# Kernel optimization log

Measured on AMD Instinct MI355X. Metric: run time of the kernel, lower is better.

The kernel has to match this reference:

```python
import jax, jax.numpy as jnp
import numpy as np
import math

D_MODEL = 1024
NUM_HEADS = 16
HEAD_DIM = D_MODEL // NUM_HEADS


def _xavier(key, out_f, in_f):
    limit = math.sqrt(6.0 / (in_f + out_f))
    return jax.random.uniform(key, (out_f, in_f), jnp.float32, -limit, limit)


def ternarize(w):
    # abs-mean threshold -> {-1, 0, +1}
    abs_mean = jnp.mean(jnp.abs(w))
    return jnp.where(jnp.abs(w) > abs_mean, jnp.sign(w), jnp.zeros_like(w))


def setup_inputs() -> dict:
    key = jax.random.key(0)
    kq, kk, kv, kwq, kwk, kwv, kwo = jax.random.split(key, 7)
    B, S = 2, 2048
    return {
        "query": jax.random.normal(kq, (B, S, D_MODEL), jnp.float32),
        "key": jax.random.normal(kk, (B, S, D_MODEL), jnp.float32),
        "value": jax.random.normal(kv, (B, S, D_MODEL), jnp.float32),
        "w_q": _xavier(kwq, D_MODEL, D_MODEL),
        "w_k": _xavier(kwk, D_MODEL, D_MODEL),
        "w_v": _xavier(kwv, D_MODEL, D_MODEL),
        "w_o": _xavier(kwo, D_MODEL, D_MODEL),
    }


def reference(query, key, value, w_q, w_k, w_v, w_o):
    B, S, _ = query.shape
    # ternary projections (F.linear: x @ W.T)
    q = query @ ternarize(w_q).T
    k = key @ ternarize(w_k).T
    v = value @ ternarize(w_v).T
    # [B, H, S, Dh]
    q = q.reshape(B, S, NUM_HEADS, HEAD_DIM).transpose(0, 2, 1, 3)
    k = k.reshape(B, -1, NUM_HEADS, HEAD_DIM).transpose(0, 2, 1, 3)
    v = v.reshape(B, -1, NUM_HEADS, HEAD_DIM).transpose(0, 2, 1, 3)
    scores = jnp.einsum("bhqd,bhkd->bhqk", q, k) / math.sqrt(HEAD_DIM)
    probs = jax.nn.softmax(scores, axis=-1)
    out = jnp.einsum("bhqk,bhkd->bhqd", probs, v)
    out = out.transpose(0, 2, 1, 3).reshape(B, S, D_MODEL)
    return out @ ternarize(w_o).T
```

## Files before the change

### kernel.cpp

```cpp
#include <hip/hip_runtime.h>
#include <cstdint>
#include <cstddef>

typedef __bf16 bfloat;
typedef __bf16 bf16x8 __attribute__((ext_vector_type(8)));
typedef __bf16 bf16x4 __attribute__((ext_vector_type(4)));
typedef float  f32x4  __attribute__((ext_vector_type(4)));

static constexpr int D  = 1024;
static constexpr int S  = 2048;
static constexpr int B  = 2;
static constexpr int H  = 16;
static constexpr int DH = 64;
static constexpr int M  = B * S;
static constexpr int WMAT_N = 1024 * 1024;

#define MFMA_BF16(a, b, c) __builtin_amdgcn_mfma_f32_16x16x32_bf16((a), (b), (c), 0, 0, 0)

__device__ __forceinline__ void gl_lds16(const void* g, void* l) {
  __builtin_amdgcn_global_load_lds(
      (const __attribute__((address_space(1))) void*)g,
      (__attribute__((address_space(3))) void*)l, 16, 0, 0);
}

__global__ void prep_kernel(const float* __restrict__ w0, const float* __restrict__ w1,
                            const float* __restrict__ w2, const float* __restrict__ w3,
                            const float* __restrict__ qx, const float* __restrict__ kx,
                            const float* __restrict__ vx, bfloat* __restrict__ qhi,
                            bfloat* __restrict__ qlo, bfloat* __restrict__ khi,
                            bfloat* __restrict__ klo, bfloat* __restrict__ vhi,
                            double* __restrict__ sums) {
  const int y = blockIdx.y;
  if (y < 4) {
    const float* w = (y == 0) ? w0 : (y == 1) ? w1 : (y == 2) ? w2 : w3;
    const float4* w4 = (const float4*)w;
    double s = 0.0;
    for (int i = blockIdx.x * blockDim.x + threadIdx.x; i < (WMAT_N / 4);
         i += gridDim.x * blockDim.x) {
      float4 v = w4[i];
      s += (double)fabsf(v.x) + (double)fabsf(v.y) + (double)fabsf(v.z) + (double)fabsf(v.w);
    }
    for (int off = 1; off < 64; off <<= 1) s += __shfl_xor(s, off, 64);
    __shared__ double ps[4];
    if ((threadIdx.x & 63) == 0) ps[threadIdx.x >> 6] = s;
    __syncthreads();
    if (threadIdx.x == 0) atomicAdd(&sums[y], ps[0] + ps[1] + ps[2] + ps[3]);
  } else {
    const int z = y - 4;
    const float* x = (z == 0) ? qx : (z == 1) ? kx : vx;
    bfloat* hi = (z == 0) ? qhi : (z == 1) ? khi : vhi;
    bfloat* lo = (z == 0) ? qlo : (z == 1) ? klo : nullptr;
    const int n8 = M * D / 8;
    const float4* x4 = (const float4*)x;
    for (int i = blockIdx.x * blockDim.x + threadIdx.x; i < n8;
         i += gridDim.x * blockDim.x) {
      float4 a = x4[2 * i], b = x4[2 * i + 1];
      float f[8] = {a.x, a.y, a.z, a.w, b.x, b.y, b.z, b.w};
      bf16x8 h;
#pragma unroll
      for (int j = 0; j < 8; j++) h[j] = (bfloat)f[j];
      *(bf16x8*)&hi[(size_t)i * 8] = h;
      if (z < 2) {
        bf16x8 l;
#pragma unroll
        for (int j = 0; j < 8; j++) l[j] = (bfloat)(f[j] - (float)h[j]);
        *(bf16x8*)&lo[(size_t)i * 8] = l;
      }
    }
  }
}

__global__ void tern_kernel(const float* __restrict__ w0, const float* __restrict__ w1,
                            const float* __restrict__ w2, const float* __restrict__ w3,
                            bfloat* __restrict__ o0, bfloat* __restrict__ o1,
                            bfloat* __restrict__ o2, bfloat* __restrict__ o3,
                            const double* __restrict__ sums) {
  int z = blockIdx.y;
  const float* w = (z == 0) ? w0 : (z == 1) ? w1 : (z == 2) ? w2 : w3;
  bfloat* o = (z == 0) ? o0 : (z == 1) ? o1 : (z == 2) ? o2 : o3;
  double thr = sums[z] * (1.0 / (double)WMAT_N);
  const float4* w4 = (const float4*)w;
  for (int i = blockIdx.x * blockDim.x + threadIdx.x; i < (WMAT_N / 4);
       i += gridDim.x * blockDim.x) {
    float4 v = w4[i];
    bf16x4 r;
    r[0] = (bfloat)(((double)fabsf(v.x) > thr) ? (v.x > 0.f ? 1.f : -1.f) : 0.f);
    r[1] = (bfloat)(((double)fabsf(v.y) > thr) ? (v.y > 0.f ? 1.f : -1.f) : 0.f);
    r[2] = (bfloat)(((double)fabsf(v.z) > thr) ? (v.z > 0.f ? 1.f : -1.f) : 0.f);
    r[3] = (bfloat)(((double)fabsf(v.w) > thr) ? (v.w > 0.f ? 1.f : -1.f) : 0.f);
    *(bf16x4*)&o[(size_t)i * 4] = r;
  }
}

__global__ __launch_bounds__(256) void qkv_gemm(
    const bfloat* __restrict__ xqh, const bfloat* __restrict__ xql,
    const bfloat* __restrict__ xkh, const bfloat* __restrict__ xkl,
    const bfloat* __restrict__ xvh, const bfloat* __restrict__ wqt,
    const bfloat* __restrict__ wkt, const bfloat* __restrict__ wvt,
    bfloat* __restrict__ qmh, bfloat* __restrict__ qml,
    bfloat* __restrict__ kmh, bfloat* __restrict__ kml, bfloat* __restrict__ vtr) {
  constexpr int K = D;
  constexpr int N = D;
  __shared__ __align__(16) bfloat As0[128 * 64];
  __shared__ __align__(16) bfloat As1[128 * 64];
  __shared__ __align__(16) bfloat Ws[128 * 64];

  const int z = blockIdx.z;
  const bfloat *A0, *A1 = nullptr, *Wm;
  bfloat *Oh = nullptr, *Ol = nullptr;
  float scale = 1.f;
  bool split;
  if (z == 0) {
    A0 = xqh; A1 = xql; Wm = wqt; Oh = qmh; Ol = qml;
    scale = 0.18033688f;
    split = true;
  } else if (z == 1) {
    A0 = xkh; A1 = xkl; Wm = wkt; Oh = kmh; Ol = kml; split = true;
  } else {
    A0 = xvh; Wm = wvt; split = false;
  }

  const int t = threadIdx.x;
  const int w = t >> 6, lane = t & 63;
  const int quad = lane >> 4, l16 = lane & 15;
  const int wm = w >> 1, wn = w & 1;
  const int m0 = blockIdx.y * 128, n0 = blockIdx.x * 128;

  f32x4 acc[4][4] = {};

  const int srr = lane >> 3;
  const int spc = lane & 7;

  for (int kk = 0; kk < K; kk += 64) {
#pragma unroll
    for (int g = 0; g < 4; g++) {
      int row = w * 32 + g * 8 + srr;
      int cl = spc ^ (row & 7);
      int lo = (w * 32 + g * 8) * 64;
      gl_lds16(A0 + (size_t)(m0 + row) * K + kk + cl * 8, As0 + lo);
      if (split) gl_lds16(A1 + (size_t)(m0 + row) * K + kk + cl * 8, As1 + lo);
      gl_lds16(Wm + (size_t)(n0 + row) * K + kk + cl * 8, Ws + lo);
    }
    __syncthreads();

#pragma unroll
    for (int kidx = 0; kidx < 2; kidx++) {
      bf16x8 bfrag[4], afrag[4];
#pragma unroll
      for (int nt = 0; nt < 4; nt++) {
        int r = wn * 64 + nt * 16 + l16;
        bfrag[nt] = *(const bf16x8*)&Ws[r * 64 + (((kidx * 4 + quad) ^ (r & 7)) * 8)];
      }
#pragma unroll
      for (int mt = 0; mt < 4; mt++) {
        int r = wm * 64 + mt * 16 + l16;
        afrag[mt] = *(const bf16x8*)&As0[r * 64 + (((kidx * 4 + quad) ^ (r & 7)) * 8)];
      }
#pragma unroll
      for (int mt = 0; mt < 4; mt++)
#pragma unroll
        for (int nt = 0; nt < 4; nt++)
          acc[mt][nt] = MFMA_BF16(afrag[mt], bfrag[nt], acc[mt][nt]);
      if (split) {
#pragma unroll
        for (int mt = 0; mt < 4; mt++) {
          int r = wm * 64 + mt * 16 + l16;
          afrag[mt] = *(const bf16x8*)&As1[r * 64 + (((kidx * 4 + quad) ^ (r & 7)) * 8)];
        }
#pragma unroll
        for (int mt = 0; mt < 4; mt++)
#pragma unroll
          for (int nt = 0; nt < 4; nt++)
            acc[mt][nt] = MFMA_BF16(afrag[mt], bfrag[nt], acc[mt][nt]);
      }
    }
    __syncthreads();
  }

#pragma unroll
  for (int mt = 0; mt < 4; mt++) {
#pragma unroll
    for (int nt = 0; nt < 4; nt++) {
      const int row = m0 + wm * 64 + mt * 16 + quad * 4;
      const int col = n0 + wn * 64 + nt * 16 + l16;
      if (split) {
#pragma unroll
        for (int rg = 0; rg < 4; rg++) {
          float vv = acc[mt][nt][rg] * scale;
          size_t idx = (size_t)(row + rg) * N + col;
          bfloat hh = (bfloat)vv;
          Oh[idx] = hh;
          Ol[idx] = (bfloat)(vv - (float)hh);
        }
      } else {
        int bb = row >> 11, s = row & (S - 1);
        bf16x4 pk;
#pragma unroll
        for (int rg = 0; rg < 4; rg++) pk[rg] = (bfloat)acc[mt][nt][rg];
        *(bf16x4*)&vtr[(size_t)bb * D * S + (size_t)col * S + s] = pk;
      }
    }
  }
}

__global__ __launch_bounds__(256, 4) void gemm_wo(const bfloat* __restrict__ A,
                                                  const bfloat* __restrict__ Wm,
                                                  float* __restrict__ Cf) {
  constexpr int K = D;
  constexpr int N = D;
  __shared__ __align__(16) bfloat As[64 * 32];
  __shared__ __align__(16) bfloat Ws[64 * 32];

  const int t = threadIdx.x;
  const int w = t >> 6, lane = t & 63;
  const int quad = lane >> 4, l16 = lane & 15;
  const int wm = w >> 1, wn = w & 1;
  const int m0 = blockIdx.y * 64, n0 = blockIdx.x * 64;

  f32x4 acc[2][2] = {};

  const int sr = w * 16 + (lane >> 2);
  const int sc = (lane & 3) ^ ((sr >> 1) & 3);

  const bfloat* pA = A + (size_t)(m0 + sr) * K + sc * 8;
  const bfloat* pW = Wm + (size_t)(n0 + sr) * K + sc * 8;
  const int ldso = w * 16 * 32;

  for (int kk = 0; kk < K; kk += 32) {
    gl_lds16(pA + kk, As + ldso);
    gl_lds16(pW + kk, Ws + ldso);
    __syncthreads();

    bf16x8 af[2], bf[2];
#pragma unroll
    for (int i = 0; i < 2; i++) {
      int ar = wm * 32 + i * 16 + l16;
      af[i] = *(const bf16x8*)&As[ar * 32 + ((quad ^ ((ar >> 1) & 3)) * 8)];
      int br = wn * 32 + i * 16 + l16;
      bf[i] = *(const bf16x8*)&Ws[br * 32 + ((quad ^ ((br >> 1) & 3)) * 8)];
    }
#pragma unroll
    for (int mt = 0; mt < 2; mt++)
#pragma unroll
      for (int nt = 0; nt < 2; nt++)
        acc[mt][nt] = MFMA_BF16(af[mt], bf[nt], acc[mt][nt]);
    __syncthreads();
  }

#pragma unroll
  for (int mt = 0; mt < 2; mt++) {
#pragma unroll
    for (int nt = 0; nt < 2; nt++) {
      const int row = m0 + wm * 32 + mt * 16 + quad * 4;
      const int col = n0 + wn * 32 + nt * 16 + l16;
#pragma unroll
      for (int rg = 0; rg < 4; rg++) Cf[(size_t)(row + rg) * N + col] = acc[mt][nt][rg];
    }
  }
}

__global__ __launch_bounds__(256) void flash_kernel(
    const bfloat* __restrict__ qh, const bfloat* __restrict__ ql,
    const bfloat* __restrict__ kh, const bfloat* __restrict__ kl,
    const bfloat* __restrict__ vt, bfloat* __restrict__ outp) {
  __shared__ __align__(16) bfloat Kh[64 * 64];
  __shared__ __align__(16) bfloat Kl[64 * 64];
  __shared__ __align__(16) bfloat Vt[64 * 64];
  __shared__ __align__(16) bfloat Pm[64 * 64];

  const int t = threadIdx.x;
  const int w = t >> 6, lane = t & 63;
  const int quad = lane >> 4, l16 = lane & 15;
  const int b = blockIdx.z, h = blockIdx.y;
  const int q0 = blockIdx.x * 64;
  const size_t base = (size_t)b * S * D + (size_t)h * DH;
  const size_t vbase = (size_t)b * D * S + (size_t)h * DH * S;

  const int ssr = lane >> 3;
  const int spc = lane & 7;

  bf16x8 ones;
#pragma unroll
  for (int j = 0; j < 8; j++) ones[j] = (bfloat)1.f;

#pragma unroll
  for (int g = 0; g < 2; g++) {
    int r = w * 16 + g * 8 + ssr;
    int c = spc ^ (r & 7);
    int lo = (w * 16 + g * 8) * 64;
    gl_lds16(qh + base + (size_t)(q0 + r) * D + c * 8, Kh + lo);
    gl_lds16(ql + base + (size_t)(q0 + r) * D + c * 8, Kl + lo);
  }
  __syncthreads();
  bf16x8 qhf[2], qlf[2];
  {
    int row = w * 16 + l16;
#pragma unroll
    for (int s2 = 0; s2 < 2; s2++) {
      qhf[s2] = *(const bf16x8*)&Kh[row * 64 + (((s2 * 4 + quad) ^ (l16 & 7)) * 8)];
      qlf[s2] = *(const bf16x8*)&Kl[row * 64 + (((s2 * 4 + quad) ^ (l16 & 7)) * 8)];
    }
  }
  __syncthreads();

  f32x4 Oa[4] = {};
  f32x4 La = {};
  float m_i = -3.0e38f;

  for (int k0 = 0; k0 < S; k0 += 64) {
#pragma unroll
    for (int g = 0; g < 2; g++) {
      int r = w * 16 + g * 8 + ssr;
      int c = spc ^ (r & 7);
      int lo = (w * 16 + g * 8) * 64;
      gl_lds16(kh + base + (size_t)(k0 + r) * D + c * 8, Kh + lo);
      gl_lds16(kl + base + (size_t)(k0 + r) * D + c * 8, Kl + lo);
      gl_lds16(vt + vbase + (size_t)r * S + k0 + c * 8, Vt + lo);
    }
    __syncthreads();

    f32x4 sf[4];
#pragma unroll
    for (int mt = 0; mt < 4; mt++) {
      f32x4 a = {};
      int krow = mt * 16 + l16;
#pragma unroll
      for (int s2 = 0; s2 < 2; s2++) {
        bf16x8 bh = *(const bf16x8*)&Kh[krow * 64 + (((s2 * 4 + quad) ^ (l16 & 7)) * 8)];
        bf16x8 bl = *(const bf16x8*)&Kl[krow * 64 + (((s2 * 4 + quad) ^ (l16 & 7)) * 8)];
        a = MFMA_BF16(bh, qhf[s2], a);
        a = MFMA_BF16(bl, qhf[s2], a);
        a = MFMA_BF16(bh, qlf[s2], a);
      }
      sf[mt] = a;
    }

    float mm = sf[0][0];
#pragma unroll
    for (int mt = 0; mt < 4; mt++)
#pragma unroll
      for (int rg = 0; rg < 4; rg++) mm = fmaxf(mm, sf[mt][rg]);
    mm = fmaxf(mm, __shfl_xor(mm, 16, 64));
    mm = fmaxf(mm, __shfl_xor(mm, 32, 64));
    if (__ballot(mm > m_i)) {
      float mnew = fmaxf(m_i, mm);
      float alpha = exp2f(m_i - mnew);
      m_i = mnew;
#pragma unroll
      for (int mt = 0; mt < 4; mt++) Oa[mt] *= alpha;
      La *= alpha;
    }
#pragma unroll
    for (int mt = 0; mt < 4; mt++)
#pragma unroll
      for (int rg = 0; rg < 4; rg++) sf[mt][rg] = exp2f(sf[mt][rg] - m_i);

#pragma unroll
    for (int mt = 0; mt < 4; mt++) {
      bf16x4 pk;
#pragma unroll
      for (int rg = 0; rg < 4; rg++) pk[rg] = (bfloat)sf[mt][rg];
      int g16 = (mt * 2 + (quad >> 1)) ^ (l16 & 7);
      *(bf16x4*)&Pm[(w * 16 + l16) * 64 + g16 * 8 + (quad & 1) * 4] = pk;
    }

#pragma unroll
    for (int s2 = 0; s2 < 2; s2++) {
      bf16x8 pb = *(const bf16x8*)&Pm[(w * 16 + l16) * 64 +
                                      (((s2 * 4 + quad) ^ (l16 & 7)) * 8)];
#pragma unroll
      for (int mt = 0; mt < 4; mt++) {
        int vrow = mt * 16 + l16;
        bf16x8 va = *(const bf16x8*)&Vt[vrow * 64 + (((s2 * 4 + quad) ^ (l16 & 7)) * 8)];
        Oa[mt] = MFMA_BF16(va, pb, Oa[mt]);
      }
      La = MFMA_BF16(ones, pb, La);
    }
    __syncthreads();
  }

  float inv = 1.0f / La[0];
  const int qrow = q0 + w * 16 + l16;
#pragma unroll
  for (int mt = 0; mt < 4; mt++) {
    bf16x4 ov;
#pragma unroll
    for (int rg = 0; rg < 4; rg++) ov[rg] = (bfloat)(Oa[mt][rg] * inv);
    *(bf16x4*)&outp[base + (size_t)qrow * D + mt * 16 + quad * 4] = ov;
  }
}

extern "C" void kernel_launch(void* const* d_in, const int* in_sizes, int n_in,
                              void* d_out, int out_size, void* d_ws, size_t ws_size,
                              hipStream_t stream) {
  const float* q_in = (const float*)d_in[0];
  const float* k_in = (const float*)d_in[1];
  const float* v_in = (const float*)d_in[2];
  const float* wq = (const float*)d_in[3];
  const float* wk = (const float*)d_in[4];
  const float* wv = (const float*)d_in[5];
  const float* wo = (const float*)d_in[6];
  float* outp = (float*)d_out;
  char* ws = (char*)d_ws;

  constexpr size_t WBYTES = (size_t)WMAT_N * 2;
  constexpr size_t XBYTES = (size_t)M * D * 2;
  size_t off = 0;
  double* sums = (double*)(ws + off); off += 256;
  bfloat* wqt = (bfloat*)(ws + off); off += WBYTES;
  bfloat* wkt = (bfloat*)(ws + off); off += WBYTES;
  bfloat* wvt = (bfloat*)(ws + off); off += WBYTES;
  bfloat* wot = (bfloat*)(ws + off); off += WBYTES;
  bfloat* xqh = (bfloat*)(ws + off); off += XBYTES;
  bfloat* xql = (bfloat*)(ws + off); off += XBYTES;
  bfloat* xkh = (bfloat*)(ws + off); off += XBYTES;
  bfloat* xkl = (bfloat*)(ws + off); off += XBYTES;
  bfloat* xvh = (bfloat*)(ws + off); off += XBYTES;
  bfloat* qmh = (bfloat*)(ws + off); off += XBYTES;
  bfloat* qml = (bfloat*)(ws + off); off += XBYTES;
  bfloat* kmh = (bfloat*)(ws + off); off += XBYTES;
  bfloat* kml = (bfloat*)(ws + off); off += XBYTES;
  bfloat* vtr = (bfloat*)(ws + off); off += XBYTES;
  bfloat* attn = xqh;

  hipMemsetAsync(sums, 0, 4 * sizeof(double), stream);
  prep_kernel<<<dim3(256, 7), 256, 0, stream>>>(
      wq, wk, wv, wo, q_in, k_in, v_in, xqh, xql, xkh, xkl, xvh, sums);
  tern_kernel<<<dim3(128, 4), 256, 0, stream>>>(wq, wk, wv, wo, wqt, wkt, wvt, wot, sums);
  qkv_gemm<<<dim3(D / 128, M / 128, 3), 256, 0, stream>>>(
      xqh, xql, xkh, xkl, xvh, wqt, wkt, wvt, qmh, qml, kmh, kml, vtr);
  flash_kernel<<<dim3(S / 64, H, B), 256, 0, stream>>>(qmh, qml, kmh, kml, vtr, attn);
  gemm_wo<<<dim3(D / 64, M / 64), 256, 0, stream>>>(attn, wot, outp);
}
```

Before: 304.6 us.

## Permute V-transpose layout to feed P from registers; widen Wo GEMM K-tile

The V projection epilogue now writes the transposed V with a permuted sequence order inside each 64-key block. This lets the flash kernel build the P operand of the PV MFMA straight from the softmax registers, dropping the LDS round trip through the Pm buffer and freeing that shared memory. Separately, the output-projection GEMM stages a 64-wide K tile with an XOR swizzle and runs two MFMA steps per barrier, which halves the synchronisation count. The permutation has to line up exactly with the MFMA register layout, so any mismatch would give wrong results.

```diff
diff --git a/kernel.cpp b/kernel.cpp
--- a/kernel.cpp
+++ b/kernel.cpp
@@ -194,10 +194,14 @@
         }
       } else {
         int bb = row >> 11, s = row & (S - 1);
+        int kk6 = s & 63;
+        int pos = (kk6 & 3) | (((kk6 >> 4) & 1) << 2) | (((kk6 >> 2) & 3) << 3) |
+                  ((kk6 >> 5) << 5);
+        int sp = (s & ~63) | pos;
         bf16x4 pk;
 #pragma unroll
         for (int rg = 0; rg < 4; rg++) pk[rg] = (bfloat)acc[mt][nt][rg];
-        *(bf16x4*)&vtr[(size_t)bb * D * S + (size_t)col * S + s] = pk;
+        *(bf16x4*)&vtr[(size_t)bb * D * S + (size_t)col * S + sp] = pk;
       }
     }
   }
@@ -208,8 +212,8 @@
                                                   float* __restrict__ Cf) {
   constexpr int K = D;
   constexpr int N = D;
-  __shared__ __align__(16) bfloat As[64 * 32];
-  __shared__ __align__(16) bfloat Ws[64 * 32];
+  __shared__ __align__(16) bfloat As[64 * 64];
+  __shared__ __align__(16) bfloat Ws[64 * 64];
 
   const int t = threadIdx.x;
   const int w = t >> 6, lane = t & 63;
@@ -219,31 +223,36 @@
 
   f32x4 acc[2][2] = {};
 
-  const int sr = w * 16 + (lane >> 2);
-  const int sc = (lane & 3) ^ ((sr >> 1) & 3);
-
-  const bfloat* pA = A + (size_t)(m0 + sr) * K + sc * 8;
-  const bfloat* pW = Wm + (size_t)(n0 + sr) * K + sc * 8;
-  const int ldso = w * 16 * 32;
-
-  for (int kk = 0; kk < K; kk += 32) {
-    gl_lds16(pA + kk, As + ldso);
-    gl_lds16(pW + kk, Ws + ldso);
-    __syncthreads();
-
-    bf16x8 af[2], bf[2];
-#pragma unroll
-    for (int i = 0; i < 2; i++) {
-      int ar = wm * 32 + i * 16 + l16;
-      af[i] = *(const bf16x8*)&As[ar * 32 + ((quad ^ ((ar >> 1) & 3)) * 8)];
-      int br = wn * 32 + i * 16 + l16;
-      bf[i] = *(const bf16x8*)&Ws[br * 32 + ((quad ^ ((br >> 1) & 3)) * 8)];
-    }
-#pragma unroll
-    for (int mt = 0; mt < 2; mt++)
-#pragma unroll
-      for (int nt = 0; nt < 2; nt++)
-        acc[mt][nt] = MFMA_BF16(af[mt], bf[nt], acc[mt][nt]);
+  const int srr = lane >> 3;
+  const int spc = lane & 7;
+
+  for (int kk = 0; kk < K; kk += 64) {
+#pragma unroll
+    for (int g = 0; g < 2; g++) {
+      int row = w * 16 + g * 8 + srr;
+      int cl = spc ^ (row & 7);
+      int lo = (w * 16 + g * 8) * 64;
+      gl_lds16(A + (size_t)(m0 + row) * K + kk + cl * 8, As + lo);
+      gl_lds16(Wm + (size_t)(n0 + row) * K + kk + cl * 8, Ws + lo);
+    }
+    __syncthreads();
+
+#pragma unroll
+    for (int kidx = 0; kidx < 2; kidx++) {
+      bf16x8 af[2], bfr[2];
+#pragma unroll
+      for (int i = 0; i < 2; i++) {
+        int ar = wm * 32 + i * 16 + l16;
+        af[i] = *(const bf16x8*)&As[ar * 64 + (((kidx * 4 + quad) ^ (ar & 7)) * 8)];
+        int br = wn * 32 + i * 16 + l16;
+        bfr[i] = *(const bf16x8*)&Ws[br * 64 + (((kidx * 4 + quad) ^ (br & 7)) * 8)];
+      }
+#pragma unroll
+      for (int mt = 0; mt < 2; mt++)
+#pragma unroll
+        for (int nt = 0; nt < 2; nt++)
+          acc[mt][nt] = MFMA_BF16(af[mt], bfr[nt], acc[mt][nt]);
+    }
     __syncthreads();
   }
 
@@ -266,7 +275,6 @@
   __shared__ __align__(16) bfloat Kh[64 * 64];
   __shared__ __align__(16) bfloat Kl[64 * 64];
   __shared__ __align__(16) bfloat Vt[64 * 64];
-  __shared__ __align__(16) bfloat Pm[64 * 64];
 
   const int t = threadIdx.x;
   const int w = t >> 6, lane = t & 63;
@@ -356,25 +364,20 @@
       for (int rg = 0; rg < 4; rg++) sf[mt][rg] = exp2f(sf[mt][rg] - m_i);
 
 #pragma unroll
-    for (int mt = 0; mt < 4; mt++) {
-      bf16x4 pk;
-#pragma unroll
-      for (int rg = 0; rg < 4; rg++) pk[rg] = (bfloat)sf[mt][rg];
-      int g16 = (mt * 2 + (quad >> 1)) ^ (l16 & 7);
-      *(bf16x4*)&Pm[(w * 16 + l16) * 64 + g16 * 8 + (quad & 1) * 4] = pk;
-    }
-
-#pragma unroll
-    for (int s2 = 0; s2 < 2; s2++) {
-      bf16x8 pb = *(const bf16x8*)&Pm[(w * 16 + l16) * 64 +
-                                      (((s2 * 4 + quad) ^ (l16 & 7)) * 8)];
+    for (int kp = 0; kp < 2; kp++) {
+      bf16x8 pb8;
+#pragma unroll
+      for (int rg = 0; rg < 4; rg++) {
+        pb8[rg]     = (bfloat)sf[2 * kp][rg];
+        pb8[4 + rg] = (bfloat)sf[2 * kp + 1][rg];
+      }
+      La = MFMA_BF16(ones, pb8, La);
 #pragma unroll
       for (int mt = 0; mt < 4; mt++) {
         int vrow = mt * 16 + l16;
-        bf16x8 va = *(const bf16x8*)&Vt[vrow * 64 + (((s2 * 4 + quad) ^ (l16 & 7)) * 8)];
-        Oa[mt] = MFMA_BF16(va, pb, Oa[mt]);
-      }
-      La = MFMA_BF16(ones, pb, La);
+        bf16x8 va = *(const bf16x8*)&Vt[vrow * 64 + (((kp * 4 + quad) ^ (vrow & 7)) * 8)];
+        Oa[mt] = MFMA_BF16(va, pb8, Oa[mt]);
+      }
     }
     __syncthreads();
   }
```

New measurement: 295.6 us. 1.03x faster.
